# Performance work log

Measured on AMD Instinct MI355X. Metric: run time of the kernel, lower is better.

The kernel has to match this reference:

```python
import jax, jax.numpy as jnp
import numpy as np

N_IN, N_UP, N_OUT = 65536, 262144, 131072
C_IN, C_OUT = 128, 64
K1, K2, K3 = 27, 27, 16      # kernel offsets: 3x3x3x1, 3x3x3x1, 2x2x2x2
M1, M2, M3 = 65536, 131072, 131072  # gather/scatter pairs per offset
EPS = 1e-6
ALPHA = 0.0


def setup_inputs() -> dict:
    key = jax.random.key(0)
    ks = jax.random.split(key, 13)
    return {
        "input_feats": jax.random.normal(ks[0], (N_IN, C_IN), jnp.float32),
        "encoder_feats": jax.random.normal(ks[1], (N_UP, C_OUT), jnp.float32),
        "W1t": jax.random.normal(ks[2], (K1, C_IN, C_OUT), jnp.float32) * 0.05,
        "W2": jax.random.normal(ks[3], (K2, C_OUT, C_OUT), jnp.float32) * 0.05,
        "W3": jax.random.normal(ks[4], (K3, C_OUT, C_OUT), jnp.float32) * 0.05,
        "Wp": jax.random.normal(ks[5], (C_OUT, 1), jnp.float32) * 0.05,
        "bp": jnp.zeros((1,), jnp.float32),
        "kin1": jax.random.randint(ks[6], (K1, M1), 0, N_IN, jnp.int32),
        "kout1": jax.random.randint(ks[7], (K1, M1), 0, N_UP, jnp.int32),
        "kin2": jax.random.randint(ks[8], (K2, M2), 0, N_UP, jnp.int32),
        "kout2": jax.random.randint(ks[9], (K2, M2), 0, N_UP, jnp.int32),
        "kin3": jax.random.randint(ks[10], (K3, M3), 0, N_UP, jnp.int32),
        "kout3": jax.random.randint(ks[11], (K3, M3), 0, N_OUT, jnp.int32),
        "n_out": N_OUT,
    }


def _sparse_conv(x, W, kin, kout, n_out):
    """Kernel-map gather-GEMM-scatter sparse conv.
    x: [N_in, Cin]; W: [K, Cin, Cout]; kin/kout: [K, M] index pairs."""
    y = jnp.einsum('kmc,kcd->kmd', x[kin], W)  # gather + per-offset GEMM
    out = jnp.zeros((n_out, W.shape[-1]), x.dtype)
    return out.at[kout].add(y)                 # scatter-accumulate


def _inorm(x):
    # MinkowskiInstanceNorm, single batch instance: per-channel over points
    mu = x.mean(0, keepdims=True)
    var = x.var(0, keepdims=True)
    return (x - mu) * jax.lax.rsqrt(var + EPS)


def reference(input_feats, encoder_feats, W1t, W2, W3, Wp, bp,
              kin1, kout1, kin2, kout2, kin3, kout3, n_out):
    n_up = encoder_feats.shape[0]
    # dec_block_1: gen conv-transpose 3x3x3x1 s2 -> IN -> ELU -> conv 3x3x3x1 -> IN -> ELU
    x = _sparse_conv(input_feats, W1t, kin1, kout1, n_up)
    x = jax.nn.elu(_inorm(x))
    x = _sparse_conv(x, W2, kin2, kout2, n_up)
    x = jax.nn.elu(_inorm(x))
    # skip connection
    x = x + encoder_feats
    # dec_block_2: conv k=2 stride [1,1,1,2] -> IN -> ELU
    x = _sparse_conv(x, W3, kin3, kout3, n_out)
    x = jax.nn.elu(_inorm(x))
    # 1x1 pruning conv (bias=True) + threshold keep mask
    pruning = x @ Wp + bp                      # [N_OUT, 1]
    keep = pruning[:, 0] > ALPHA
    # MinkowskiPruning gathers kept rows (dynamic shape); static-shape
    # equivalent: zero out pruned rows and return the mask.
    return x * keep[:, None].astype(x.dtype), keep
```

## Files before the change

kernel.cpp:

```cpp
#include <hip/hip_runtime.h>
#include <math.h>

#define N_IN   65536
#define N_UP   262144
#define N_OUT  131072
#define C_IN   128
#define C_OUT  64
#define K1     27
#define K2     27
#define K3     16
#define M1     65536
#define M2     131072
#define M3     131072
#define EPSV   1e-6f
#define WPK    256
#define WPK_SHIFT 8

template <int CIN, int MSHIFT>
__global__ __launch_bounds__(256) void conv_gemm(
    const float* __restrict__ X, const float* __restrict__ W,
    const int* __restrict__ kin, const int* __restrict__ kout,
    float* __restrict__ outp)
{
    __shared__ float lds_t[4][64][20];
    __shared__ int   lds_dst[4][64];

    const int lane = threadIdx.x & 63;
    const int wv   = threadIdx.x >> 6;
    const int wave = blockIdx.x * 4 + wv;
    const int k    = __builtin_amdgcn_readfirstlane(wave >> WPK_SHIFT);
    const int widx = wave & (WPK - 1);
    constexpr int R  = (1 << MSHIFT) / WPK;
    constexpr int NB = R / 64;
    constexpr int KC = CIN / 16;

    const float* Wk = W + (size_t)k * (CIN * 64);
    const int base = (k << MSHIFT) + widx * R;

    for (int b = 0; b < NB; ++b) {
        const int j   = base + b * 64 + lane;
        const int src = kin[j];
        const int dst = kout[j];
        lds_dst[wv][lane] = dst;

        const float4* xr = (const float4*)(X + (size_t)src * CIN);

        float acc[64];
#pragma unroll
        for (int c = 0; c < 64; ++c) acc[c] = 0.f;

        float4 xa0 = xr[0], xa1 = xr[1], xa2 = xr[2], xa3 = xr[3];

        for (int kc = 0; kc < KC; ++kc) {
            float4 xb0, xb1, xb2, xb3;
            if (kc + 1 < KC) {
                xb0 = xr[(kc + 1) * 4 + 0];
                xb1 = xr[(kc + 1) * 4 + 1];
                xb2 = xr[(kc + 1) * 4 + 2];
                xb3 = xr[(kc + 1) * 4 + 3];
            }
            float xs[16];
            xs[0]=xa0.x; xs[1]=xa0.y; xs[2]=xa0.z; xs[3]=xa0.w;
            xs[4]=xa1.x; xs[5]=xa1.y; xs[6]=xa1.z; xs[7]=xa1.w;
            xs[8]=xa2.x; xs[9]=xa2.y; xs[10]=xa2.z; xs[11]=xa2.w;
            xs[12]=xa3.x; xs[13]=xa3.y; xs[14]=xa3.z; xs[15]=xa3.w;

            const float* wrow = Wk + kc * 16 * 64;
#pragma unroll
            for (int i = 0; i < 16; ++i) {
                const float xi = xs[i];
                const float* wr = wrow + i * 64;
#pragma unroll
                for (int c = 0; c < 64; ++c)
                    acc[c] = fmaf(xi, wr[c], acc[c]);
            }
            xa0 = xb0; xa1 = xb1; xa2 = xb2; xa3 = xb3;
        }

#pragma unroll
        for (int cc = 0; cc < 4; ++cc) {
#pragma unroll
            for (int q = 0; q < 4; ++q) {
                float4 v;
                v.x = acc[cc * 16 + q * 4 + 0];
                v.y = acc[cc * 16 + q * 4 + 1];
                v.z = acc[cc * 16 + q * 4 + 2];
                v.w = acc[cc * 16 + q * 4 + 3];
                *(float4*)&lds_t[wv][lane][q * 4] = v;
            }
            const int c16 = lane & 15;
#pragma unroll
            for (int t = 0; t < 16; ++t) {
                const int rr = (lane >> 4) + 4 * t;
                const float v = lds_t[wv][rr][c16];
                const int   d = lds_dst[wv][rr];
                atomicAdd(outp + (size_t)d * 64 + cc * 16 + c16, v);
            }
        }
    }
}

__global__ __launch_bounds__(256) void stats_kernel(
    const float* __restrict__ x, int nrows, float* __restrict__ stats)
{
    __shared__ float sh[2][4][64];
    const int c  = threadIdx.x & 63;
    const int rw = threadIdx.x >> 6;
    float s = 0.f, s2 = 0.f;
    for (int r = blockIdx.x * 4 + rw; r < nrows; r += gridDim.x * 4) {
        float v = x[(size_t)r * 64 + c];
        s += v;
        s2 = fmaf(v, v, s2);
    }
    sh[0][rw][c] = s;
    sh[1][rw][c] = s2;
    __syncthreads();
    if (rw == 0) {
        s  = (sh[0][0][c] + sh[0][1][c]) + (sh[0][2][c] + sh[0][3][c]);
        s2 = (sh[1][0][c] + sh[1][1][c]) + (sh[1][2][c] + sh[1][3][c]);
        atomicAdd(stats + c, s);
        atomicAdd(stats + 64 + c, s2);
    }
}

__global__ void finalize_stats(float* stats, float inv_n)
{
    const int c = threadIdx.x;
    float mu  = stats[c] * inv_n;
    float var = stats[64 + c] * inv_n - mu * mu;
    stats[128 + c] = mu;
    stats[192 + c] = rsqrtf(var + EPSV);
}

__global__ __launch_bounds__(256) void norm_elu(
    float* __restrict__ x, const float* __restrict__ stats,
    const float* __restrict__ enc)
{
    const int i = blockIdx.x * 256 + threadIdx.x;
    const int c = i & 63;
    float v = (x[i] - stats[128 + c]) * stats[192 + c];
    v = (v > 0.f) ? v : expm1f(v);
    if (enc) v += enc[i];
    x[i] = v;
}

__global__ __launch_bounds__(256) void final_kernel(
    const float* __restrict__ x, const float* __restrict__ stats,
    const float* __restrict__ Wp, const float* __restrict__ bp,
    float* __restrict__ outp)
{
    const int lane = threadIdx.x & 63;
    const int wid  = threadIdx.x >> 6;
    const int row  = blockIdx.x * 4 + wid;

    float v = (x[(size_t)row * 64 + lane] - stats[128 + lane]) * stats[192 + lane];
    v = (v > 0.f) ? v : expm1f(v);

    float p = v * Wp[lane];
#pragma unroll
    for (int m = 1; m < 64; m <<= 1)
        p += __shfl_xor(p, m, 64);
    p += bp[0];

    const bool keep = p > 0.0f;
    outp[(size_t)row * 64 + lane] = keep ? v : 0.f;
    if (lane == 0)
        outp[(size_t)N_OUT * 64 + row] = keep ? 1.f : 0.f;
}

extern "C" void kernel_launch(void* const* d_in, const int* in_sizes, int n_in,
                              void* d_out, int out_size, void* d_ws, size_t ws_size,
                              hipStream_t stream)
{
    const float* in_feats = (const float*)d_in[0];
    const float* enc      = (const float*)d_in[1];
    const float* W1       = (const float*)d_in[2];
    const float* W2       = (const float*)d_in[3];
    const float* W3       = (const float*)d_in[4];
    const float* Wp       = (const float*)d_in[5];
    const float* bp       = (const float*)d_in[6];
    const int* kin1  = (const int*)d_in[7];
    const int* kout1 = (const int*)d_in[8];
    const int* kin2  = (const int*)d_in[9];
    const int* kout2 = (const int*)d_in[10];
    const int* kin3  = (const int*)d_in[11];
    const int* kout3 = (const int*)d_in[12];
    float* outp = (float*)d_out;

    char* ws = (char*)d_ws;
    float* up_a   = (float*)ws;
    float* up_b   = (float*)(ws + 67108864);
    float* out3   = up_a;
    float* statsA = (float*)(ws + 134217728);
    float* statsB = statsA + 256;
    float* statsC = statsA + 512;

    hipMemsetAsync(up_a, 0, (size_t)N_UP * 64 * 4, stream);
    hipMemsetAsync(up_b, 0, (size_t)N_UP * 64 * 4, stream);
    hipMemsetAsync(statsA, 0, 3 * 256 * 4, stream);

    conv_gemm<128, 16><<<(K1 * WPK) / 4, 256, 0, stream>>>(
        in_feats, W1, kin1, kout1, up_a);
    stats_kernel<<<512, 256, 0, stream>>>(up_a, N_UP, statsA);
    finalize_stats<<<1, 64, 0, stream>>>(statsA, 1.f / N_UP);
    norm_elu<<<(N_UP * 64) / 256, 256, 0, stream>>>(up_a, statsA, nullptr);

    conv_gemm<64, 17><<<(K2 * WPK) / 4, 256, 0, stream>>>(
        up_a, W2, kin2, kout2, up_b);
    stats_kernel<<<512, 256, 0, stream>>>(up_b, N_UP, statsB);
    finalize_stats<<<1, 64, 0, stream>>>(statsB, 1.f / N_UP);
    norm_elu<<<(N_UP * 64) / 256, 256, 0, stream>>>(up_b, statsB, enc);

    hipMemsetAsync(out3, 0, (size_t)N_OUT * 64 * 4, stream);
    conv_gemm<64, 17><<<(K3 * WPK) / 4, 256, 0, stream>>>(
        up_b, W3, kin3, kout3, out3);
    stats_kernel<<<512, 256, 0, stream>>>(out3, N_OUT, statsC);
    finalize_stats<<<1, 64, 0, stream>>>(statsC, 1.f / N_OUT);

    final_kernel<<<N_OUT / 4, 256, 0, stream>>>(out3, statsC, Wp, bp, outp);
}
```

Baseline: 2.505 ms.

## Bucket kernel-map pairs by output tile and accumulate in LDS instead of global atomics

Adds a counting sort (histogram, scan, scatter) that groups gather/scatter pairs by 256-row output tile and offset, packing source index and local row into one word. Each block then owns one output tile, accumulates contributions with LDS atomics using a rotated column layout to spread banks, and writes the tile once. This removes the global float atomics and the full-buffer memsets, and deepens X prefetch to two chunks. In exchange it adds three preprocessing kernels per conv, including a single-block scan, plus per-element global atomics on the bucket cursors. Per-bucket work is imbalanced, and the sort scratch is borrowed from the output buffer.

```diff
diff --git a/kernel.cpp b/kernel.cpp
--- a/kernel.cpp
+++ b/kernel.cpp
@@ -9,94 +9,154 @@
 #define K1     27
 #define K2     27
 #define K3     16
-#define M1     65536
-#define M2     131072
-#define M3     131072
 #define EPSV   1e-6f
-#define WPK    256
-#define WPK_SHIFT 8
-
-template <int CIN, int MSHIFT>
-__global__ __launch_bounds__(256) void conv_gemm(
+#define TSHIFT 8
+
+template <int KNUM, int MSHIFT>
+__global__ __launch_bounds__(256) void hist_kernel(
+    const int* __restrict__ kout, int* __restrict__ hist)
+{
+    const int n = KNUM << MSHIFT;
+    for (int j = blockIdx.x * 256 + threadIdx.x; j < n; j += gridDim.x * 256) {
+        const int k = j >> MSHIFT;
+        const int b = kout[j] >> TSHIFT;
+        atomicAdd(hist + b * KNUM + k, 1);
+    }
+}
+
+__global__ __launch_bounds__(1024) void scan_kernel(
+    const int* __restrict__ hist, int* __restrict__ offs,
+    int* __restrict__ cursor, int nbins)
+{
+    __shared__ int ps[1024];
+    const int t = threadIdx.x;
+    const int per = (nbins + 1023) >> 10;
+    const int base = t * per;
+    int s = 0;
+    for (int i = 0; i < per; ++i) {
+        const int b = base + i;
+        if (b < nbins) s += hist[b];
+    }
+    ps[t] = s;
+    __syncthreads();
+    for (int off = 1; off < 1024; off <<= 1) {
+        const int v = (t >= off) ? ps[t - off] : 0;
+        __syncthreads();
+        ps[t] += v;
+        __syncthreads();
+    }
+    int run = (t == 0) ? 0 : ps[t - 1];
+    for (int i = 0; i < per; ++i) {
+        const int b = base + i;
+        if (b < nbins) {
+            const int h = hist[b];
+            offs[b] = run;
+            cursor[b] = run;
+            run += h;
+        }
+    }
+    if (t == 1023) offs[nbins] = run;
+}
+
+template <int KNUM, int MSHIFT>
+__global__ __launch_bounds__(256) void scatter_kernel(
+    const int* __restrict__ kin, const int* __restrict__ kout,
+    int* __restrict__ cursor, unsigned* __restrict__ sorted)
+{
+    const int n = KNUM << MSHIFT;
+    for (int j = blockIdx.x * 256 + threadIdx.x; j < n; j += gridDim.x * 256) {
+        const int k   = j >> MSHIFT;
+        const int dst = kout[j];
+        const int b   = dst >> TSHIFT;
+        const int pos = atomicAdd(cursor + b * KNUM + k, 1);
+        sorted[pos] = (unsigned)kin[j] |
+                      ((unsigned)(dst & ((1 << TSHIFT) - 1)) << 18);
+    }
+}
+
+template <int CIN, int KNUM>
+__global__ __launch_bounds__(256) void conv_tile(
     const float* __restrict__ X, const float* __restrict__ W,
-    const int* __restrict__ kin, const int* __restrict__ kout,
+    const unsigned* __restrict__ sorted, const int* __restrict__ offs,
     float* __restrict__ outp)
 {
-    __shared__ float lds_t[4][64][20];
-    __shared__ int   lds_dst[4][64];
-
-    const int lane = threadIdx.x & 63;
-    const int wv   = threadIdx.x >> 6;
-    const int wave = blockIdx.x * 4 + wv;
-    const int k    = __builtin_amdgcn_readfirstlane(wave >> WPK_SHIFT);
-    const int widx = wave & (WPK - 1);
-    constexpr int R  = (1 << MSHIFT) / WPK;
-    constexpr int NB = R / 64;
+    __shared__ float tile[256][64];
+    const int lane   = threadIdx.x & 63;
+    const int wv     = threadIdx.x >> 6;
+    const int bucket = blockIdx.x;
     constexpr int KC = CIN / 16;
 
-    const float* Wk = W + (size_t)k * (CIN * 64);
-    const int base = (k << MSHIFT) + widx * R;
-
-    for (int b = 0; b < NB; ++b) {
-        const int j   = base + b * 64 + lane;
-        const int src = kin[j];
-        const int dst = kout[j];
-        lds_dst[wv][lane] = dst;
-
-        const float4* xr = (const float4*)(X + (size_t)src * CIN);
-
-        float acc[64];
-#pragma unroll
-        for (int c = 0; c < 64; ++c) acc[c] = 0.f;
-
-        float4 xa0 = xr[0], xa1 = xr[1], xa2 = xr[2], xa3 = xr[3];
-
-        for (int kc = 0; kc < KC; ++kc) {
-            float4 xb0, xb1, xb2, xb3;
-            if (kc + 1 < KC) {
-                xb0 = xr[(kc + 1) * 4 + 0];
-                xb1 = xr[(kc + 1) * 4 + 1];
-                xb2 = xr[(kc + 1) * 4 + 2];
-                xb3 = xr[(kc + 1) * 4 + 3];
+    float4* tf = (float4*)&tile[0][0];
+#pragma unroll
+    for (int i = 0; i < 16; ++i)
+        tf[threadIdx.x + 256 * i] = float4{0.f, 0.f, 0.f, 0.f};
+    __syncthreads();
+
+    for (int k = wv; k < KNUM; k += 4) {
+        const int s = offs[bucket * KNUM + k];
+        const int e = offs[bucket * KNUM + k + 1];
+        const float* Wk = W +
+            (size_t)__builtin_amdgcn_readfirstlane(k) * (CIN * 64);
+
+        for (int bs = s; bs < e; bs += 64) {
+            const int idx    = bs + lane;
+            const bool valid = idx < e;
+            const unsigned word = valid ? sorted[idx] : 0u;
+            const int src = word & 0x3FFFF;
+            const int rl  = word >> 18;
+
+            const float4* xr = (const float4*)(X + (size_t)src * CIN);
+
+            float acc[64];
+#pragma unroll
+            for (int c = 0; c < 64; ++c) acc[c] = 0.f;
+
+            float4 xa0 = xr[0], xa1 = xr[1], xa2 = xr[2], xa3 = xr[3];
+            float4 xb0 = xr[4], xb1 = xr[5], xb2 = xr[6], xb3 = xr[7];
+
+            for (int kc = 0; kc < KC; ++kc) {
+                float4 xc0, xc1, xc2, xc3;
+                if (kc + 2 < KC) {
+                    xc0 = xr[(kc + 2) * 4 + 0];
+                    xc1 = xr[(kc + 2) * 4 + 1];
+                    xc2 = xr[(kc + 2) * 4 + 2];
+                    xc3 = xr[(kc + 2) * 4 + 3];
+                } else {
+                    xc0 = xa0; xc1 = xa1; xc2 = xa2; xc3 = xa3;
+                }
+
+                float xs[16];
+                xs[0]=xa0.x; xs[1]=xa0.y; xs[2]=xa0.z; xs[3]=xa0.w;
+                xs[4]=xa1.x; xs[5]=xa1.y; xs[6]=xa1.z; xs[7]=xa1.w;
+                xs[8]=xa2.x; xs[9]=xa2.y; xs[10]=xa2.z; xs[11]=xa2.w;
+                xs[12]=xa3.x; xs[13]=xa3.y; xs[14]=xa3.z; xs[15]=xa3.w;
+
+                const float* wrow = Wk + kc * 16 * 64;
+#pragma unroll
+                for (int i = 0; i < 16; ++i) {
+                    const float xi = xs[i];
+                    const float* wr = wrow + i * 64;
+#pragma unroll
+                    for (int c = 0; c < 64; ++c)
+                        acc[c] = fmaf(xi, wr[c], acc[c]);
+                }
+                xa0 = xb0; xa1 = xb1; xa2 = xb2; xa3 = xb3;
+                xb0 = xc0; xb1 = xc1; xb2 = xc2; xb3 = xc3;
             }
-            float xs[16];
-            xs[0]=xa0.x; xs[1]=xa0.y; xs[2]=xa0.z; xs[3]=xa0.w;
-            xs[4]=xa1.x; xs[5]=xa1.y; xs[6]=xa1.z; xs[7]=xa1.w;
-            xs[8]=xa2.x; xs[9]=xa2.y; xs[10]=xa2.z; xs[11]=xa2.w;
-            xs[12]=xa3.x; xs[13]=xa3.y; xs[14]=xa3.z; xs[15]=xa3.w;
-
-            const float* wrow = Wk + kc * 16 * 64;
-#pragma unroll
-            for (int i = 0; i < 16; ++i) {
-                const float xi = xs[i];
-                const float* wr = wrow + i * 64;
+
+            if (valid) {
 #pragma unroll
                 for (int c = 0; c < 64; ++c)
-                    acc[c] = fmaf(xi, wr[c], acc[c]);
-            }
-            xa0 = xb0; xa1 = xb1; xa2 = xb2; xa3 = xb3;
-        }
-
-#pragma unroll
-        for (int cc = 0; cc < 4; ++cc) {
-#pragma unroll
-            for (int q = 0; q < 4; ++q) {
-                float4 v;
-                v.x = acc[cc * 16 + q * 4 + 0];
-                v.y = acc[cc * 16 + q * 4 + 1];
-                v.z = acc[cc * 16 + q * 4 + 2];
-                v.w = acc[cc * 16 + q * 4 + 3];
-                *(float4*)&lds_t[wv][lane][q * 4] = v;
-            }
-            const int c16 = lane & 15;
-#pragma unroll
-            for (int t = 0; t < 16; ++t) {
-                const int rr = (lane >> 4) + 4 * t;
-                const float v = lds_t[wv][rr][c16];
-                const int   d = lds_dst[wv][rr];
-                atomicAdd(outp + (size_t)d * 64 + cc * 16 + c16, v);
+                    atomicAdd(&tile[rl][(c + rl) & 63], acc[c]);
             }
         }
+    }
+    __syncthreads();
+
+    const int rbase = wv * 64;
+    for (int r = rbase; r < rbase + 64; ++r) {
+        const float v = tile[r][(lane + r) & 63];
+        outp[((size_t)(bucket << TSHIFT) + r) * 64 + lane] = v;
     }
 }
 
@@ -195,25 +255,42 @@
     float* statsB = statsA + 256;
     float* statsC = statsA + 512;
 
-    hipMemsetAsync(up_a, 0, (size_t)N_UP * 64 * 4, stream);
-    hipMemsetAsync(up_b, 0, (size_t)N_UP * 64 * 4, stream);
-    hipMemsetAsync(statsA, 0, 3 * 256 * 4, stream);
-
-    conv_gemm<128, 16><<<(K1 * WPK) / 4, 256, 0, stream>>>(
-        in_feats, W1, kin1, kout1, up_a);
+    char* scratch = (char*)d_out;
+    unsigned* sorted = (unsigned*)scratch;
+    int* hist   = (int*)(scratch + 16777216);
+    int* offs   = (int*)(scratch + 16908288);
+    int* cursor = (int*)(scratch + 17039360);
+
+    const int NBK1 = N_UP  >> TSHIFT;
+    const int NBK3 = N_OUT >> TSHIFT;
+    const int NB1  = NBK1 * K1;
+    const int NB3  = NBK3 * K3;
+
+    (void)hipMemsetAsync(statsA, 0, 3 * 256 * 4, stream);
+
+    (void)hipMemsetAsync(hist, 0, NB1 * 4, stream);
+    hist_kernel<K1, 16><<<1024, 256, 0, stream>>>(kout1, hist);
+    scan_kernel<<<1, 1024, 0, stream>>>(hist, offs, cursor, NB1);
+    scatter_kernel<K1, 16><<<1024, 256, 0, stream>>>(kin1, kout1, cursor, sorted);
+    conv_tile<128, K1><<<NBK1, 256, 0, stream>>>(in_feats, W1, sorted, offs, up_a);
     stats_kernel<<<512, 256, 0, stream>>>(up_a, N_UP, statsA);
     finalize_stats<<<1, 64, 0, stream>>>(statsA, 1.f / N_UP);
     norm_elu<<<(N_UP * 64) / 256, 256, 0, stream>>>(up_a, statsA, nullptr);
 
-    conv_gemm<64, 17><<<(K2 * WPK) / 4, 256, 0, stream>>>(
-        up_a, W2, kin2, kout2, up_b);
+    (void)hipMemsetAsync(hist, 0, NB1 * 4, stream);
+    hist_kernel<K2, 17><<<1024, 256, 0, stream>>>(kout2, hist);
+    scan_kernel<<<1, 1024, 0, stream>>>(hist, offs, cursor, NB1);
+    scatter_kernel<K2, 17><<<1024, 256, 0, stream>>>(kin2, kout2, cursor, sorted);
+    conv_tile<64, K2><<<NBK1, 256, 0, stream>>>(up_a, W2, sorted, offs, up_b);
     stats_kernel<<<512, 256, 0, stream>>>(up_b, N_UP, statsB);
     finalize_stats<<<1, 64, 0, stream>>>(statsB, 1.f / N_UP);
     norm_elu<<<(N_UP * 64) / 256, 256, 0, stream>>>(up_b, statsB, enc);
 
-    hipMemsetAsync(out3, 0, (size_t)N_OUT * 64 * 4, stream);
-    conv_gemm<64, 17><<<(K3 * WPK) / 4, 256, 0, stream>>>(
-        up_b, W3, kin3, kout3, out3);
+    (void)hipMemsetAsync(hist, 0, NB3 * 4, stream);
+    hist_kernel<K3, 17><<<1024, 256, 0, stream>>>(kout3, hist);
+    scan_kernel<<<1, 1024, 0, stream>>>(hist, offs, cursor, NB3);
+    scatter_kernel<K3, 17><<<1024, 256, 0, stream>>>(kin3, kout3, cursor, sorted);
+    conv_tile<64, K3><<<NBK3, 256, 0, stream>>>(up_b, W3, sorted, offs, out3);
     stats_kernel<<<512, 256, 0, stream>>>(out3, N_OUT, statsC);
     finalize_stats<<<1, 64, 0, stream>>>(statsC, 1.f / N_OUT);
 
```

New measurement: 5.198 ms. 2.07x slower.
